# Kernel tuning notes

Hardware: AMD Instinct MI355X
Metric: run time of the kernel (lower is better)

Reference implementation:

```python
import jax, jax.numpy as jnp
import numpy as np

# reformer-enwik8-style config (trimmed to 2 layers, 2 hash rounds)
B, S, D = 2, 4096, 1024          # batch, seq, hidden
H, Dh = 8, 128                   # heads, head dim (H*Dh == D)
R, C, NB = 2, 64, 128            # num hashes, lsh chunk len, num buckets
L, FF, V = 2, 4096, 258          # layers, ffn dim, vocab
EPS = 1e-12
CAUSAL_NEG, SELF_NEG = -1e9, -1e5


def layer_norm(x, g, b):
    mu = x.mean(-1, keepdims=True)
    var = ((x - mu) ** 2).mean(-1, keepdims=True)
    return (x - mu) * jax.lax.rsqrt(var + EPS) * g + b


def lsh_attn(h, Wqk, Wv, Wo, rot):
    # shared query/key projection (Reformer LSH uses tied Q=K)
    qk = (h @ Wqk).reshape(B, S, H, Dh).transpose(0, 2, 1, 3)   # [B,H,S,Dh]
    v = (h @ Wv).reshape(B, S, H, Dh).transpose(0, 2, 1, 3)
    # LSH bucketing via random rotations: rot [H,Dh,R,NB//2]
    rotated = jnp.einsum('bhsd,hdrn->bhrsn', qk, rot)
    buckets = jnp.argmax(jnp.concatenate([rotated, -rotated], -1), axis=-1)  # [B,H,R,S]
    ids = (buckets + jnp.arange(R)[None, None, :, None] * NB).reshape(B, H, R * S)
    pos = jnp.tile(jnp.arange(S), R)
    # stable sort by (bucket, position)
    sticker = jnp.argsort(ids * S + pos[None, None, :], axis=-1)  # [B,H,R*S]
    orig = sticker % S
    gather = lambda t: jnp.take_along_axis(t, orig[..., None], axis=2)
    sq = gather(qk)                                               # [B,H,RS,Dh]
    sv = gather(v)
    # key = len-normalized qk / sqrt(Dh) (HF _len_and_dim_norm)
    sk = sq * jax.lax.rsqrt(jnp.mean(sq * sq, -1, keepdims=True) + 1e-6) / jnp.sqrt(float(Dh))
    nc = R * S // C
    qc = sq.reshape(B, H, nc, C, Dh)
    kc = sk.reshape(B, H, nc, C, Dh)
    vc = sv.reshape(B, H, nc, C, Dh)
    pc = orig.reshape(B, H, nc, C)
    # attend to current chunk + 1 previous chunk (wraparound, as in HF)
    ke = jnp.concatenate([jnp.roll(kc, 1, axis=2), kc], axis=3)   # [B,H,nc,2C,Dh]
    ve = jnp.concatenate([jnp.roll(vc, 1, axis=2), vc], axis=3)
    pe = jnp.concatenate([jnp.roll(pc, 1, axis=2), pc], axis=3)   # [B,H,nc,2C]
    scores = jnp.einsum('bhncd,bhnkd->bhnck', qc, ke)
    qpos, kpos = pc[..., :, None], pe[..., None, :]
    scores = jnp.where(kpos > qpos, CAUSAL_NEG, scores)           # causal (decoder)
    scores = jnp.where(kpos == qpos, SELF_NEG, scores)            # mask self (q==k)
    lse = jax.scipy.special.logsumexp(scores, axis=-1, keepdims=True)
    probs = jnp.exp(scores - lse)
    o = jnp.einsum('bhnck,bhnkd->bhncd', probs, ve).reshape(B, H, R * S, Dh)
    lg = lse.reshape(B, H, R * S)
    undo = jnp.argsort(sticker, axis=-1)
    o = jnp.take_along_axis(o, undo[..., None], axis=2).reshape(B, H, R, S, Dh)
    lg = jnp.take_along_axis(lg, undo, axis=2).reshape(B, H, R, S)
    # combine hash rounds weighted by their logsumexp
    w = jax.nn.softmax(lg, axis=2)[..., None]
    out = (o * w).sum(2)                                          # [B,H,S,Dh]
    out = out.transpose(0, 2, 1, 3).reshape(B, S, H * Dh)
    return out @ Wo


def _forward(x, ln1_g, ln1_b, Wqk, Wv, Wo, rot, ln2_g, ln2_b, W1, b1, W2, b2,
             lnf_g, lnf_b, Wout, bout):
    # reversible residual encoder: x1,x2 start as duplicated hidden states
    x1 = x2 = x
    for l in range(L):
        x1 = x1 + lsh_attn(layer_norm(x2, ln1_g[l], ln1_b[l]), Wqk[l], Wv[l], Wo[l], rot[l])
        x2 = x2 + jax.nn.relu(layer_norm(x1, ln2_g[l], ln2_b[l]) @ W1[l] + b1[l]) @ W2[l] + b2[l]
    hcat = layer_norm(jnp.concatenate([x1, x2], -1), lnf_g, lnf_b)  # [B,S,2D]
    logits = hcat @ Wout + bout
    # F.softmax(x) with no dim on a 3D tensor -> legacy torch dim=0
    return jax.nn.softmax(logits, axis=0)


def setup_inputs() -> dict:
    key = jax.random.key(0)
    ks = jax.random.split(key, 8)
    s = 0.02
    return {
        'x': jax.random.normal(ks[0], (B, S, D), jnp.float32),
        'ln1_g': jnp.ones((L, D), jnp.float32), 'ln1_b': jnp.zeros((L, D), jnp.float32),
        'Wqk': jax.random.normal(ks[1], (L, D, H * Dh), jnp.float32) * s,
        'Wv': jax.random.normal(ks[2], (L, D, H * Dh), jnp.float32) * s,
        'Wo': jax.random.normal(ks[3], (L, H * Dh, D), jnp.float32) * s,
        'rot': jax.random.normal(ks[4], (L, H, Dh, R, NB // 2), jnp.float32),
        'ln2_g': jnp.ones((L, D), jnp.float32), 'ln2_b': jnp.zeros((L, D), jnp.float32),
        'W1': jax.random.normal(ks[5], (L, D, FF), jnp.float32) * s,
        'b1': jnp.zeros((L, FF), jnp.float32),
        'W2': jax.random.normal(ks[6], (L, FF, D), jnp.float32) * s,
        'b2': jnp.zeros((L, D), jnp.float32),
        'lnf_g': jnp.ones((2 * D,), jnp.float32), 'lnf_b': jnp.zeros((2 * D,), jnp.float32),
        'Wout': jax.random.normal(ks[7], (2 * D, V), jnp.float32) * s,
        'bout': jnp.zeros((V,), jnp.float32),
    }


def reference(x, ln1_g, ln1_b, Wqk, Wv, Wo, rot, ln2_g, ln2_b, W1, b1, W2, b2,
              lnf_g, lnf_b, Wout, bout):
    return _forward(x, ln1_g, ln1_b, Wqk, Wv, Wo, rot, ln2_g, ln2_b, W1, b1, W2, b2,
                    lnf_g, lnf_b, Wout, bout)
```

## Files before the change

### kernel.cpp

```cpp
#include <hip/hip_runtime.h>
#include <hip/hip_fp16.h>
#include <math.h>

#define BB 2
#define SS 4096
#define DD 1024
#define HH 8
#define DH 128
#define RR 2
#define CC 64
#define NBUCK 128
#define LL 2
#define FFD 4096
#define VV 258
#define VP 384
#define RS (RR*SS)
#define NC (RS/CC)
#define BH (BB*HH)
#define MROWS (BB*SS)

#define SCF 256.0f
#define DSCF (1.0f/65536.0f)

typedef __attribute__((ext_vector_type(8))) _Float16 v8h;
typedef __attribute__((ext_vector_type(4))) _Float16 v4h;
typedef __attribute__((ext_vector_type(4))) float v4f;

__device__ __forceinline__ void gld16(const void* g, void* l) {
  __builtin_amdgcn_global_load_lds((const __attribute__((address_space(1))) void*)g,
                                   (__attribute__((address_space(3))) void*)l, 16, 0, 0);
}

__device__ __forceinline__ void block_sum2(float& s, float& s2) {
  #pragma unroll
  for (int o = 1; o < 64; o <<= 1) { s += __shfl_xor(s, o); s2 += __shfl_xor(s2, o); }
  __shared__ float rs[4], rq[4];
  int wave = threadIdx.x >> 6;
  if ((threadIdx.x & 63) == 0) { rs[wave] = s; rq[wave] = s2; }
  __syncthreads();
  s  = rs[0] + rs[1] + rs[2] + rs[3];
  s2 = rq[0] + rq[1] + rq[2] + rq[3];
}

__global__ __launch_bounds__(256) void init_x_kernel(const float* __restrict__ x,
                                                     float* __restrict__ x1,
                                                     float* __restrict__ x2) {
  size_t i = (size_t)blockIdx.x * 256 + threadIdx.x;
  float v = x[i];
  x1[i] = v; x2[i] = v;
}

__global__ __launch_bounds__(256) void ln_split_kernel(const float* __restrict__ x,
                                                       const float* __restrict__ g,
                                                       const float* __restrict__ bta,
                                                       _Float16* __restrict__ out) {
  int row = blockIdx.x;
  int t = threadIdx.x;
  float4 xv = ((const float4*)(x + (size_t)row * DD))[t];
  float s  = xv.x + xv.y + xv.z + xv.w;
  float s2 = xv.x*xv.x + xv.y*xv.y + xv.z*xv.z + xv.w*xv.w;
  block_sum2(s, s2);
  float mu   = s * (1.0f / DD);
  float var  = fmaxf(s2 * (1.0f / DD) - mu * mu, 0.0f);
  float rstd = rsqrtf(var + 1e-12f);
  float4 gv = ((const float4*)g)[t];
  float4 bv = ((const float4*)bta)[t];
  float4 sv;
  sv.x = ((xv.x - mu) * rstd * gv.x + bv.x) * SCF;
  sv.y = ((xv.y - mu) * rstd * gv.y + bv.y) * SCF;
  sv.z = ((xv.z - mu) * rstd * gv.z + bv.z) * SCF;
  sv.w = ((xv.w - mu) * rstd * gv.w + bv.w) * SCF;
  v4h h0, h1;
  h0[0]=(_Float16)sv.x; h0[1]=(_Float16)sv.y; h0[2]=(_Float16)sv.z; h0[3]=(_Float16)sv.w;
  h1[0]=(_Float16)(sv.x-(float)h0[0]); h1[1]=(_Float16)(sv.y-(float)h0[1]);
  h1[2]=(_Float16)(sv.z-(float)h0[2]); h1[3]=(_Float16)(sv.w-(float)h0[3]);
  const size_t PLN = (size_t)MROWS * DD;
  size_t base = (size_t)row * DD + t * 4;
  *(v4h*)(out + base) = h0;
  *(v4h*)(out + PLN + base) = h1;
}

__global__ __launch_bounds__(256) void ln_concat_split_kernel(const float* __restrict__ x1,
                                                              const float* __restrict__ x2,
                                                              const float* __restrict__ g,
                                                              const float* __restrict__ bta,
                                                              _Float16* __restrict__ out) {
  int row = blockIdx.x;
  int t = threadIdx.x;
  float4 a = ((const float4*)(x1 + (size_t)row * DD))[t];
  float4 b = ((const float4*)(x2 + (size_t)row * DD))[t];
  float s  = a.x + a.y + a.z + a.w + b.x + b.y + b.z + b.w;
  float s2 = a.x*a.x + a.y*a.y + a.z*a.z + a.w*a.w
           + b.x*b.x + b.y*b.y + b.z*b.z + b.w*b.w;
  block_sum2(s, s2);
  float mu   = s * (1.0f / (2*DD));
  float var  = fmaxf(s2 * (1.0f / (2*DD)) - mu * mu, 0.0f);
  float rstd = rsqrtf(var + 1e-12f);
  float4 g1 = ((const float4*)g)[t];
  float4 b1v = ((const float4*)bta)[t];
  float4 g2 = ((const float4*)g)[256 + t];
  float4 b2v = ((const float4*)bta)[256 + t];
  const size_t PLN = (size_t)MROWS * (2*DD);
  float4 s1, s2v;
  s1.x = ((a.x-mu)*rstd*g1.x + b1v.x)*SCF;  s1.y = ((a.y-mu)*rstd*g1.y + b1v.y)*SCF;
  s1.z = ((a.z-mu)*rstd*g1.z + b1v.z)*SCF;  s1.w = ((a.w-mu)*rstd*g1.w + b1v.w)*SCF;
  s2v.x = ((b.x-mu)*rstd*g2.x + b2v.x)*SCF; s2v.y = ((b.y-mu)*rstd*g2.y + b2v.y)*SCF;
  s2v.z = ((b.z-mu)*rstd*g2.z + b2v.z)*SCF; s2v.w = ((b.w-mu)*rstd*g2.w + b2v.w)*SCF;
  v4h h0, h1;
  size_t base = (size_t)row * (2*DD) + t * 4;
  h0[0]=(_Float16)s1.x; h0[1]=(_Float16)s1.y; h0[2]=(_Float16)s1.z; h0[3]=(_Float16)s1.w;
  h1[0]=(_Float16)(s1.x-(float)h0[0]); h1[1]=(_Float16)(s1.y-(float)h0[1]);
  h1[2]=(_Float16)(s1.z-(float)h0[2]); h1[3]=(_Float16)(s1.w-(float)h0[3]);
  *(v4h*)(out + base) = h0;
  *(v4h*)(out + PLN + base) = h1;
  h0[0]=(_Float16)s2v.x; h0[1]=(_Float16)s2v.y; h0[2]=(_Float16)s2v.z; h0[3]=(_Float16)s2v.w;
  h1[0]=(_Float16)(s2v.x-(float)h0[0]); h1[1]=(_Float16)(s2v.y-(float)h0[1]);
  h1[2]=(_Float16)(s2v.z-(float)h0[2]); h1[3]=(_Float16)(s2v.w-(float)h0[3]);
  *(v4h*)(out + base + DD) = h0;
  *(v4h*)(out + PLN + base + DD) = h1;
}

__global__ __launch_bounds__(256) void wconv_kernel(const float* __restrict__ W,
                                                    _Float16* __restrict__ Wt,
                                                    int K, int N, int Npad, int ldw) {
  __shared__ float tile[32][33];
  int n0 = blockIdx.x * 32, k0 = blockIdx.y * 32;
  int tid = threadIdx.x;
  #pragma unroll
  for (int i = 0; i < 4; i++) {
    int idx = i*256 + tid;
    int kk = idx >> 5, nn = idx & 31;
    float v = 0.0f;
    if (n0 + nn < N) v = W[(size_t)(k0 + kk) * ldw + n0 + nn];
    tile[kk][nn] = v;
  }
  __syncthreads();
  size_t NKs = (size_t)Npad * K;
  #pragma unroll
  for (int i = 0; i < 4; i++) {
    int idx = i*256 + tid;
    int nn = idx >> 5, kk = idx & 31;
    float s = tile[kk][nn] * SCF;
    size_t off = (size_t)(n0 + nn) * K + k0 + kk;
    _Float16 h0 = (_Float16)s;
    _Float16 h1 = (_Float16)(s - (float)h0);
    Wt[off] = h0;
    Wt[NKs + off] = h1;
  }
}

template<int PL, int CMODE, bool BIAS, bool RELU, int NP>
__global__ __launch_bounds__(256) void qgemm_kernel(const _Float16* __restrict__ A,
                                                    const _Float16* __restrict__ Bt,
                                                    const float* __restrict__ bias,
                                                    void* __restrict__ Cv,
                                                    int M, int N, int K,
                                                    size_t aplane, size_t bplane) {
  __shared__ __align__(16) _Float16 As[2*128*32];
  __shared__ __align__(16) _Float16 Bs[2*128*32];
  int tid = threadIdx.x, lane = tid & 63, wave = tid >> 6;
  int m0 = blockIdx.y * 128, n0 = blockIdx.x * 128;
  int wm = (wave & 1) * 64, wn = (wave >> 1) * 64;
  int lm = lane & 15, quad = lane >> 4;
  const int NCH = (PL == 2) ? 8 : 4;
  const int ACH = (PL == 2) ? 16 : 8;
  v4f acc[4][4];
  #pragma unroll
  for (int i = 0; i < 4; i++)
    #pragma unroll
    for (int j = 0; j < 4; j++) acc[i][j] = (v4f)0.0f;

  for (int k0 = 0; k0 < K; k0 += 32) {
    #pragma unroll
    for (int i = 0; i < NCH; i++) {
      int c = wave * NCH + i;
      if (c < ACH) {
        int p = c >> 3, q = c & 7;
        int row = q * 16 + (lane >> 2), col = (lane & 3) * 8;
        gld16(A + (size_t)p * aplane + (size_t)(m0 + row) * K + k0 + col,
              (char*)As + (size_t)c * 1024);
      } else {
        int cb = c - ACH;
        int p = cb >> 3, q = cb & 7;
        int row = q * 16 + (lane >> 2), col = (lane & 3) * 8;
        gld16(Bt + (size_t)p * bplane + (size_t)(n0 + row) * K + k0 + col,
              (char*)Bs + (size_t)cb * 1024);
      }
    }
    __syncthreads();
    v8h a[4][2], b[4][2];
    #pragma unroll
    for (int ni = 0; ni < 4; ni++) {
      int boff = (wn + ni*16 + lm) * 32 + quad * 8;
      b[ni][0] = *(const v8h*)&Bs[boff];
      if (PL == 2) b[ni][1] = *(const v8h*)&Bs[4096 + boff];
    }
    #pragma unroll
    for (int mi = 0; mi < 4; mi++) {
      int aoff = (wm + mi*16 + lm) * 32 + quad * 8;
      a[mi][0] = *(const v8h*)&As[aoff];
      if (PL == 2) a[mi][1] = *(const v8h*)&As[4096 + aoff];
    }
    #pragma unroll
    for (int mi = 0; mi < 4; mi++) {
      #pragma unroll
      for (int ni = 0; ni < 4; ni++) {
        v4f c0 = acc[mi][ni];
        c0 = __builtin_amdgcn_mfma_f32_16x16x32_f16(a[mi][0], b[ni][0], c0, 0, 0, 0);
        if (PL == 2) {
          c0 = __builtin_amdgcn_mfma_f32_16x16x32_f16(a[mi][0], b[ni][1], c0, 0, 0, 0);
          c0 = __builtin_amdgcn_mfma_f32_16x16x32_f16(a[mi][1], b[ni][0], c0, 0, 0, 0);
          if (NP == 4)
            c0 = __builtin_amdgcn_mfma_f32_16x16x32_f16(a[mi][1], b[ni][1], c0, 0, 0, 0);
        }
        acc[mi][ni] = c0;
      }
    }
    __syncthreads();
  }

  float* Cf = (float*)Cv;
  _Float16* Ch = (_Float16*)Cv;
  const size_t cplane = (size_t)M * N;
  #pragma unroll
  for (int mi = 0; mi < 4; mi++) {
    int rbase = m0 + wm + mi*16 + quad*4;
    #pragma unroll
    for (int ni = 0; ni < 4; ni++) {
      int col = n0 + wn + ni*16 + lm;
      float bv = BIAS ? bias[col] : 0.0f;
      #pragma unroll
      for (int r = 0; r < 4; r++) {
        float val = acc[mi][ni][r] * DSCF + bv;
        if (RELU) val = fmaxf(val, 0.0f);
        size_t off = (size_t)(rbase + r) * N + col;
        if (CMODE == 0) Cf[off] = val;
        else if (CMODE == 1) Cf[off] += val;
        else {
          float s = val * SCF;
          _Float16 h0 = (_Float16)s;
          _Float16 h1 = (_Float16)(s - (float)h0);
          Ch[off] = h0;
          Ch[cplane + off] = h1;
        }
      }
    }
  }
}

__global__ __launch_bounds__(256) void rott_kernel(const float* __restrict__ rot,
                                                   _Float16* __restrict__ rotT) {
  int h = blockIdx.x, grp = blockIdx.y;
  const float* rh = rot + (size_t)h * (DH * RR * 64);
  for (int idx = threadIdx.x; idx < 16*128; idx += 256) {
    int rc = grp*16 + (idx >> 7), d = idx & 127;
    int r = rc >> 6, nn = rc & 63;
    float f = rh[(size_t)d * 128 + r * 64 + nn] * SCF;
    _Float16 h0 = (_Float16)f;
    rotT[(size_t)h*32768 + (size_t)rc*128 + d] = h0;
    rotT[(size_t)h*32768 + 16384 + (size_t)rc*128 + d] = (_Float16)(f - (float)h0);
  }
}

__global__ __launch_bounds__(256) void bucket_mfma_kernel(const float* __restrict__ qkb,
                                                          const _Float16* __restrict__ rotT,
                                                          int* __restrict__ ids) {
  __shared__ __align__(16) float Af[128*32];
  __shared__ __align__(16) _Float16 Bs[2*128*32];
  int mtile = blockIdx.x, bh = blockIdx.y;
  int b = bh >> 3, h = bh & 7;
  int tid = threadIdx.x, lane = tid & 63, wave = tid >> 6;
  int wm = (wave & 1) * 64;
  int r = wave >> 1;
  int wn = r * 64;
  int lm = lane & 15, quad = lane >> 4;
  const float* Aq = qkb + ((size_t)b * SS + (size_t)mtile * 128) * DD + h * DH;
  const _Float16* Bq = rotT + (size_t)h * 32768;
  v4f acc[4][4];
  #pragma unroll
  for (int i = 0; i < 4; i++)
    #pragma unroll
    for (int j = 0; j < 4; j++) acc[i][j] = (v4f)0.0f;

  for (int k0 = 0; k0 < 128; k0 += 32) {
    #pragma unroll
    for (int i = 0; i < 8; i++) {
      int c = wave * 8 + i;
      if (c < 16) {
        int slot = c * 64 + lane;
        int row = slot >> 3;
        int c4 = (slot & 7) ^ (row & 7);
        gld16(Aq + (size_t)row * DD + k0 + c4 * 4, (char*)Af + (size_t)c * 1024);
      } else {
        int cb = c - 16;
        int p = cb >> 3, q = cb & 7;
        int row = q * 16 + (lane >> 2), col = (lane & 3) * 8;
        gld16(Bq + (size_t)p * 16384 + (size_t)row * 128 + k0 + col,
              (char*)Bs + (size_t)p * 8192 + (size_t)q * 1024);
      }
    }
    __syncthreads();
    v8h b0[4], b1[4];
    #pragma unroll
    for (int ni = 0; ni < 4; ni++) {
      int boff = (wn + ni*16 + lm) * 32 + quad * 8;
      b0[ni] = *(const v8h*)&Bs[boff];
      b1[ni] = *(const v8h*)&Bs[4096 + boff];
    }
    #pragma unroll
    for (int mi = 0; mi < 4; mi++) {
      int arow = wm + mi*16 + lm;
      int sw = arow & 7;
      float4 fA = *(const float4*)(Af + arow*32 + (((2*quad)     ^ sw) << 2));
      float4 fB = *(const float4*)(Af + arow*32 + (((2*quad + 1) ^ sw) << 2));
      v8h a0, a1;
      float fs[8] = {fA.x*SCF, fA.y*SCF, fA.z*SCF, fA.w*SCF,
                     fB.x*SCF, fB.y*SCF, fB.z*SCF, fB.w*SCF};
      #pragma unroll
      for (int j = 0; j < 8; j++) {
        _Float16 p0 = (_Float16)fs[j];
        a0[j] = p0;
        a1[j] = (_Float16)(fs[j] - (float)p0);
      }
      #pragma unroll
      for (int ni = 0; ni < 4; ni++) {
        v4f c0 = acc[mi][ni];
        c0 = __builtin_amdgcn_mfma_f32_16x16x32_f16(a0, b0[ni], c0, 0, 0, 0);
        c0 = __builtin_amdgcn_mfma_f32_16x16x32_f16(a0, b1[ni], c0, 0, 0, 0);
        c0 = __builtin_amdgcn_mfma_f32_16x16x32_f16(a1, b0[ni], c0, 0, 0, 0);
        c0 = __builtin_amdgcn_mfma_f32_16x16x32_f16(a1, b1[ni], c0, 0, 0, 0);
        acc[mi][ni] = c0;
      }
    }
    __syncthreads();
  }

  #pragma unroll
  for (int mi = 0; mi < 4; mi++) {
    #pragma unroll
    for (int rr = 0; rr < 4; rr++) {
      float mx = acc[mi][0][rr]; int xi = lm;
      float mn = acc[mi][0][rr]; int ni_ = lm;
      #pragma unroll
      for (int ni = 1; ni < 4; ni++) {
        float vv = acc[mi][ni][rr];
        int col = ni*16 + lm;
        if (vv > mx) { mx = vv; xi = col; }
        if (vv < mn) { mn = vv; ni_ = col; }
      }
      #pragma unroll
      for (int o = 1; o < 16; o <<= 1) {
        float ox = __shfl_xor(mx, o); int oxi = __shfl_xor(xi, o);
        if (ox > mx || (ox == mx && oxi < xi)) { mx = ox; xi = oxi; }
        float on = __shfl_xor(mn, o); int oni = __shfl_xor(ni_, o);
        if (on < mn || (on == mn && oni < ni_)) { mn = on; ni_ = oni; }
      }
      if (lm == 0) {
        int bi = (mx >= -mn) ? xi : 64 + ni_;
        int s = mtile*128 + wm + mi*16 + quad*4 + rr;
        ids[((size_t)bh * RR + r) * SS + s] = bi + r * NBUCK;
      }
    }
  }
}

__global__ __launch_bounds__(256) void sort_count_kernel(const int* __restrict__ ids,
                                                         int* __restrict__ counts) {
  int w = blockIdx.x * 4 + (threadIdx.x >> 6);
  int lane = threadIdx.x & 63;
  int bhr = w >> 6, seg = w & 63;
  int id = ids[(size_t)bhr * SS + seg * 64 + lane];
  int bin = id & 127;
  unsigned long long eq = ~0ull;
  #pragma unroll
  for (int bit = 0; bit < 7; bit++) {
    unsigned long long bal = __ballot((bin >> bit) & 1);
    eq &= ((bin >> bit) & 1) ? bal : ~bal;
  }
  int rank = __popcll(eq & ((1ull << lane) - 1ull));
  if (rank == 0)
    counts[((size_t)bhr * 64 + seg) * 128 + bin] = __popcll(eq);
}

__global__ __launch_bounds__(128) void sort_prefix_kernel(int* __restrict__ counts) {
  int bhr = blockIdx.x;
  int bin = threadIdx.x;
  int r = bhr & 1;
  int* cp = counts + (size_t)bhr * 64 * 128;
  int total = 0;
  for (int seg = 0; seg < 64; seg++) total += cp[seg * 128 + bin];
  __shared__ int tot[128];
  tot[bin] = total;
  __syncthreads();
  for (int off = 1; off < 128; off <<= 1) {
    int t = (bin >= off) ? tot[bin - off] : 0;
    __syncthreads();
    tot[bin] += t;
    __syncthreads();
  }
  int run = tot[bin] - total + r * SS;
  for (int seg = 0; seg < 64; seg++) {
    int c = cp[seg * 128 + bin];
    cp[seg * 128 + bin] = run;
    run += c;
  }
}

__global__ __launch_bounds__(256) void sort_scatter_kernel(const int* __restrict__ ids,
                                                           const int* __restrict__ offs,
                                                           int* __restrict__ orig,
                                                           int* __restrict__ undo) {
  int w = blockIdx.x * 4 + (threadIdx.x >> 6);
  int lane = threadIdx.x & 63;
  int bhr = w >> 6, seg = w & 63;
  int s = seg * 64 + lane;
  int id = ids[(size_t)bhr * SS + s];
  int bin = id & 127;
  unsigned long long eq = ~0ull;
  #pragma unroll
  for (int bit = 0; bit < 7; bit++) {
    unsigned long long bal = __ballot((bin >> bit) & 1);
    eq &= ((bin >> bit) & 1) ? bal : ~bal;
  }
  int rank = __popcll(eq & ((1ull << lane) - 1ull));
  int o = offs[((size_t)bhr * 64 + seg) * 128 + bin] + rank;
  int bh = bhr >> 1, r = bhr & 1;
  orig[(size_t)bh * RS + o] = s;
  undo[(size_t)bh * RS + r * SS + s] = o;
}

__global__ __launch_bounds__(256) void rnorm_kernel(const float* __restrict__ qk,
                                                    const int* __restrict__ orig,
                                                    float* __restrict__ rno) {
  int idx = blockIdx.x * 4 + (threadIdx.x >> 6);
  int lane = threadIdx.x & 63;
  int bh = idx >> 13;
  int k = idx & (RS - 1);
  int b = bh >> 3, h = bh & 7;
  int s = orig[(size_t)bh * RS + k];
  const float* row = qk + ((size_t)(b * SS + s)) * DD + h * DH;
  float x0 = row[lane], x1 = row[lane + 64];
  float ss = x0 * x0 + x1 * x1;
  #pragma unroll
  for (int o = 1; o < 64; o <<= 1) ss += __shfl_xor(ss, o);
  if (lane == 0)
    rno[(size_t)bh * RS + k] = rsqrtf(ss * (1.0f / DH) + 1e-6f) * 0.08838834764831845f;
}

template<int PL>
__global__ __launch_bounds__(256) void attn_mfma_kernel(const float* __restrict__ qk,
                                                        const float* __restrict__ v,
                                                        const int* __restrict__ orig,
                                                        const float* __restrict__ rno,
                                                        float* __restrict__ osort,
                                                        float* __restrict__ lg) {
  constexpr int QPs = 64*136, Kps = 32*136, Vps = 128*36;
  constexpr size_t QPB = (size_t)PL * QPs * 2;
  constexpr size_t KVB = (size_t)PL * Vps * 2;
  __shared__ __align__(16) char smem[QPB + KVB + 1024];
  _Float16* QP = (_Float16*)smem;
  _Float16* KV = (_Float16*)(smem + QPB);
  int* kp_lds = (int*)(smem + QPB + KVB);
  int* qp_lds = kp_lds + 128;

  int blk = blockIdx.x;
  int n = blk & (NC - 1), bh = blk >> 7;
  int b = bh >> 3, h = bh & 7;
  int pn = (n + NC - 1) & (NC - 1);
  int tid = threadIdx.x, lane = tid & 63, wave = tid >> 6;
  int lm = lane & 15, quad = lane >> 4;
  const int* origp = orig + (size_t)bh * RS;
  const float* rnp = rno + (size_t)bh * RS;
  const size_t base = (size_t)b * SS * DD + (size_t)h * DH;

  for (int idx = tid; idx < 64*32; idx += 256) {
    int q = idx >> 5, d4 = idx & 31;
    float4 f = *(const float4*)(qk + base + (size_t)origp[n*64+q]*DD + d4*4);
    f.x *= SCF; f.y *= SCF; f.z *= SCF; f.w *= SCF;
    v4h h0; h0[0]=(_Float16)f.x; h0[1]=(_Float16)f.y; h0[2]=(_Float16)f.z; h0[3]=(_Float16)f.w;
    *(v4h*)(QP + q*136 + d4*4) = h0;
    if (PL == 2) {
      v4h h1; h1[0]=(_Float16)(f.x-(float)h0[0]); h1[1]=(_Float16)(f.y-(float)h0[1]);
      h1[2]=(_Float16)(f.z-(float)h0[2]); h1[3]=(_Float16)(f.w-(float)h0[3]);
      *(v4h*)(QP + QPs + q*136 + d4*4) = h1;
    }
  }
  if (tid < 128) kp_lds[tid] = origp[(tid < 64) ? (pn*64 + tid) : (n*64 + tid - 64)];
  else if (tid < 192) qp_lds[tid - 128] = origp[n*64 + tid - 128];

  v4f sc[8];
  #pragma unroll
  for (int j = 0; j < 8; j++) sc[j] = (v4f)0.0f;

  #pragma unroll
  for (int g = 0; g < 4; g++) {
    __syncthreads();
    for (int idx = tid; idx < 32*32; idx += 256) {
      int key = idx >> 5, d4 = idx & 31;
      int kidx = ((g < 2) ? (pn*64 + g*32) : (n*64 + (g-2)*32)) + key;
      float rn = rnp[kidx] * SCF;
      float4 f = *(const float4*)(qk + base + (size_t)origp[kidx]*DD + d4*4);
      f.x *= rn; f.y *= rn; f.z *= rn; f.w *= rn;
      v4h h0; h0[0]=(_Float16)f.x; h0[1]=(_Float16)f.y; h0[2]=(_Float16)f.z; h0[3]=(_Float16)f.w;
      *(v4h*)(KV + key*136 + d4*4) = h0;
      if (PL == 2) {
        v4h h1; h1[0]=(_Float16)(f.x-(float)h0[0]); h1[1]=(_Float16)(f.y-(float)h0[1]);
        h1[2]=(_Float16)(f.z-(float)h0[2]); h1[3]=(_Float16)(f.w-(float)h0[3]);
        *(v4h*)(KV + Kps + key*136 + d4*4) = h1;
      }
    }
    __syncthreads();
    #pragma unroll
    for (int ni = 0; ni < 2; ni++) {
      v4f c0 = sc[g*2 + ni];
      #pragma unroll
      for (int ks = 0; ks < 4; ks++) {
        v8h a0 = *(const v8h*)(QP + (wave*16 + lm)*136 + ks*32 + quad*8);
        v8h b0 = *(const v8h*)(KV + (ni*16 + lm)*136 + ks*32 + quad*8);
        c0 = __builtin_amdgcn_mfma_f32_16x16x32_f16(a0, b0, c0, 0, 0, 0);
        if (PL == 2) {
          v8h a1 = *(const v8h*)(QP + QPs + (wave*16 + lm)*136 + ks*32 + quad*8);
          v8h b1 = *(const v8h*)(KV + Kps + (ni*16 + lm)*136 + ks*32 + quad*8);
          c0 = __builtin_amdgcn_mfma_f32_16x16x32_f16(a0, b1, c0, 0, 0, 0);
          c0 = __builtin_amdgcn_mfma_f32_16x16x32_f16(a1, b0, c0, 0, 0, 0);
          c0 = __builtin_amdgcn_mfma_f32_16x16x32_f16(a1, b1, c0, 0, 0, 0);
        }
      }
      sc[g*2 + ni] = c0;
    }
  }
  __syncthreads();

  int kp_l[8];
  #pragma unroll
  for (int j = 0; j < 8; j++) kp_l[j] = kp_lds[j*16 + lm];

  #pragma unroll
  for (int rr = 0; rr < 4; rr++) {
    int row = wave*16 + quad*4 + rr;
    int qp = qp_lds[row];
    float sv[8];
    #pragma unroll
    for (int j = 0; j < 8; j++) {
      float s = sc[j][rr] * DSCF;
      int kp = kp_l[j];
      sv[j] = (kp > qp) ? -1000000000.0f : ((kp == qp) ? -100000.0f : s);
    }
    float m = sv[0];
    #pragma unroll
    for (int j = 1; j < 8; j++) m = fmaxf(m, sv[j]);
    #pragma unroll
    for (int o = 1; o < 16; o <<= 1) m = fmaxf(m, __shfl_xor(m, o));
    float es[8], S = 0.0f;
    #pragma unroll
    for (int j = 0; j < 8; j++) { es[j] = __expf(sv[j] - m); S += es[j]; }
    #pragma unroll
    for (int o = 1; o < 16; o <<= 1) S += __shfl_xor(S, o);
    float inv = 1.0f / S;
    if (lm == 0) lg[(size_t)bh * RS + n*64 + row] = m + __logf(S);
    #pragma unroll
    for (int j = 0; j < 8; j++) {
      float p = es[j] * inv * SCF;
      _Float16 p0 = (_Float16)p;
      QP[row*136 + j*16 + lm] = p0;
      if (PL == 2) QP[QPs + row*136 + j*16 + lm] = (_Float16)(p - (float)p0);
    }
  }

  v4f oacc[8];
  #pragma unroll
  for (int j = 0; j < 8; j++) oacc[j] = (v4f)0.0f;
  #pragma unroll
  for (int g = 0; g < 4; g++) {
    __syncthreads();
    for (int idx = tid; idx < 32*32; idx += 256) {
      int key = idx >> 5, d4 = idx & 31;
      int kidx = ((g < 2) ? (pn*64 + g*32) : (n*64 + (g-2)*32)) + key;
      float4 f = *(const float4*)(v + base + (size_t)origp[kidx]*DD + d4*4);
      float fs[4] = {f.x*SCF, f.y*SCF, f.z*SCF, f.w*SCF};
      #pragma unroll
      for (int j = 0; j < 4; j++) {
        int d = d4*4 + j;
        _Float16 p0 = (_Float16)fs[j];
        KV[d*36 + key] = p0;
        if (PL == 2) KV[Vps + d*36 + key] = (_Float16)(fs[j] - (float)p0);
      }
    }
    __syncthreads();
    v8h a0 = *(const v8h*)(QP + (wave*16 + lm)*136 + g*32 + quad*8);
    v8h a1;
    if (PL == 2) a1 = *(const v8h*)(QP + QPs + (wave*16 + lm)*136 + g*32 + quad*8);
    #pragma unroll
    for (int dn = 0; dn < 8; dn++) {
      v4h lo0 = *(const v4h*)(KV + (dn*16 + lm)*36 + quad*8);
      v4h hi0 = *(const v4h*)(KV + (dn*16 + lm)*36 + quad*8 + 4);
      v8h b0 = __builtin_shufflevector(lo0, hi0, 0,1,2,3,4,5,6,7);
      v4f c0 = oacc[dn];
      c0 = __builtin_amdgcn_mfma_f32_16x16x32_f16(a0, b0, c0, 0, 0, 0);
      if (PL == 2) {
        v4h lo1 = *(const v4h*)(KV + Vps + (dn*16 + lm)*36 + quad*8);
        v4h hi1 = *(const v4h*)(KV + Vps + (dn*16 + lm)*36 + quad*8 + 4);
        v8h b1 = __builtin_shufflevector(lo1, hi1, 0,1,2,3,4,5,6,7);
        c0 = __builtin_amdgcn_mfma_f32_16x16x32_f16(a0, b1, c0, 0, 0, 0);
        c0 = __builtin_amdgcn_mfma_f32_16x16x32_f16(a1, b0, c0, 0, 0, 0);
        c0 = __builtin_amdgcn_mfma_f32_16x16x32_f16(a1, b1, c0, 0, 0, 0);
      }
      oacc[dn] = c0;
    }
  }

  #pragma unroll
  for (int dn = 0; dn < 8; dn++) {
    #pragma unroll
    for (int rr = 0; rr < 4; rr++) {
      int row = wave*16 + quad*4 + rr;
      osort[((size_t)bh * RS + n*64 + row) * DH + dn*16 + lm] = oacc[dn][rr] * DSCF;
    }
  }
}

__global__ __launch_bounds__(256) void unsort_split_kernel(const float* __restrict__ osort,
                                                           const float* __restrict__ lg,
                                                           const int* __restrict__ undo,
                                                           _Float16* __restrict__ attn) {
  int gid = blockIdx.x * 4 + (threadIdx.x >> 6);
  int lane = threadIdx.x & 63;
  int bh = gid >> 12;
  int s = gid & (SS - 1);
  int b = bh >> 3, h = bh & 7;
  int k0 = undo[(size_t)bh * RS + s];
  int k1 = undo[(size_t)bh * RS + SS + s];
  float l0 = lg[(size_t)bh * RS + k0], l1 = lg[(size_t)bh * RS + k1];
  float m = fmaxf(l0, l1);
  float e0 = __expf(l0 - m), e1 = __expf(l1 - m);
  float inv = 1.0f / (e0 + e1);
  float w0 = e0 * inv, w1 = e1 * inv;
  const float* r0 = osort + ((size_t)bh * RS + k0) * DH;
  const float* r1 = osort + ((size_t)bh * RS + k1) * DH;
  const size_t PLN = (size_t)MROWS * DD;
  _Float16* outp = attn + ((size_t)(b * SS + s)) * DD + h * DH;
  float sA = (w0 * r0[lane]      + w1 * r1[lane])      * SCF;
  float sB = (w0 * r0[lane + 64] + w1 * r1[lane + 64]) * SCF;
  _Float16 a0 = (_Float16)sA, b0 = (_Float16)sB;
  outp[lane] = a0;                 outp[lane + 64] = b0;
  outp[PLN + lane] = (_Float16)(sA - (float)a0);
  outp[PLN + lane + 64] = (_Float16)(sB - (float)b0);
}

__global__ __launch_bounds__(256) void softmax_b_kernel(const float* __restrict__ logits,
                                                        const float* __restrict__ bout,
                                                        float* __restrict__ out) {
  int i = blockIdx.x * 256 + threadIdx.x;
  if (i >= SS * VV) return;
  int s = i / VV, vv = i - s * VV;
  float bvv = bout[vv];
  float l0 = logits[(size_t)s * VP + vv] + bvv;
  float l1 = logits[(size_t)(SS + s) * VP + vv] + bvv;
  float m = fmaxf(l0, l1);
  float e0 = __expf(l0 - m), e1 = __expf(l1 - m);
  float inv = 1.0f / (e0 + e1);
  out[(size_t)s * VV + vv] = e0 * inv;
  out[(size_t)(SS + s) * VV + vv] = e1 * inv;
}

extern "C" void kernel_launch(void* const* d_in, const int* in_sizes, int n_in,
                              void* d_out, int out_size, void* d_ws, size_t ws_size,
                              hipStream_t stream) {
  (void)in_sizes; (void)n_in; (void)out_size; (void)ws_size;
  const float* x     = (const float*)d_in[0];
  const float* ln1_g = (const float*)d_in[1];
  const float* ln1_b = (const float*)d_in[2];
  const float* Wqk   = (const float*)d_in[3];
  const float* Wv    = (const float*)d_in[4];
  const float* Wo    = (const float*)d_in[5];
  const float* rot   = (const float*)d_in[6];
  const float* ln2_g = (const float*)d_in[7];
  const float* ln2_b = (const float*)d_in[8];
  const float* W1    = (const float*)d_in[9];
  const float* b1    = (const float*)d_in[10];
  const float* W2    = (const float*)d_in[11];
  const float* b2    = (const float*)d_in[12];
  const float* lnf_g = (const float*)d_in[13];
  const float* lnf_b = (const float*)d_in[14];
  const float* Wout  = (const float*)d_in[15];
  const float* bout  = (const float*)d_in[16];

  const size_t NX = (size_t)MROWS * DD;
  float* x1 = (float*)d_ws;
  float* x2 = x1 + NX;
  float* h  = x2 + NX;
  _Float16* hs = (_Float16*)h;
  float* pool = h + NX;
  float* qkb   = pool;
  float* vb    = pool + NX;
  float* osort = pool + 2*NX;
  _Float16* ffh = (_Float16*)pool;
  _Float16* hcs = (_Float16*)pool;
  char* wbase = (char*)(pool + 2*NX);
  _Float16* wt = (_Float16*)wbase;
  int* counts = (int*)(wbase + (8u<<20));
  _Float16* rotTs = (_Float16*)(wbase + (10u<<20));
  float* after = pool + 4*NX;
  float* lgb = after;
  float* rno = lgb + (size_t)BH * RS;
  int* orig = (int*)(rno + (size_t)BH * RS);
  int* undo = orig + (size_t)BH * RS;
  int* ids  = undo + (size_t)BH * RS;
  float* logitsP = h;

  const size_t AP_D  = NX;
  const size_t AP_FF = (size_t)MROWS * 2048;
  const size_t BP_D  = (size_t)DD * DD;
  const size_t BP_W1 = (size_t)2048 * DD;
  const size_t BP_W2 = (size_t)DD * 2048;
  const size_t BP_HD = (size_t)VP * 2048;

  init_x_kernel<<<(int)(NX / 256), 256, 0, stream>>>(x, x1, x2);

  for (int l = 0; l < LL; l++) {
    ln_split_kernel<<<MROWS, 256, 0, stream>>>(x2, ln1_g + l*DD, ln1_b + l*DD, hs);

    wconv_kernel<<<dim3(32, 32), 256, 0, stream>>>(Wqk + (size_t)l*DD*DD, wt, DD, DD, DD, DD);
    qgemm_kernel<2,0,false,false,4><<<dim3(8, 64), 256, 0, stream>>>(
        hs, wt, nullptr, qkb, MROWS, DD, DD, AP_D, BP_D);

    wconv_kernel<<<dim3(32, 32), 256, 0, stream>>>(Wv + (size_t)l*DD*DD, wt, DD, DD, DD, DD);
    if (l == 0)
      qgemm_kernel<2,0,false,false,3><<<dim3(8, 64), 256, 0, stream>>>(
          hs, wt, nullptr, vb, MROWS, DD, DD, AP_D, BP_D);
    else
      qgemm_kernel<1,0,false,false,3><<<dim3(8, 64), 256, 0, stream>>>(
          hs, wt, nullptr, vb, MROWS, DD, DD, AP_D, BP_D);

    rott_kernel<<<dim3(8, 8), 256, 0, stream>>>(rot + (size_t)l*HH*DH*RR*64, rotTs);
    bucket_mfma_kernel<<<dim3(32, 16), 256, 0, stream>>>(qkb, rotTs, ids);

    hipMemsetAsync(counts, 0, (size_t)BH * RR * 64 * 128 * sizeof(int), stream);
    sort_count_kernel<<<512, 256, 0, stream>>>(ids, counts);
    sort_prefix_kernel<<<BH*RR, 128, 0, stream>>>(counts);
    sort_scatter_kernel<<<512, 256, 0, stream>>>(ids, counts, orig, undo);

    rnorm_kernel<<<BH*RS/4, 256, 0, stream>>>(qkb, orig, rno);
    if (l == 0)
      attn_mfma_kernel<2><<<BH*NC, 256, 0, stream>>>(qkb, vb, orig, rno, osort, lgb);
    else
      attn_mfma_kernel<1><<<BH*NC, 256, 0, stream>>>(qkb, vb, orig, rno, osort, lgb);
    unsort_split_kernel<<<BH*SS/4, 256, 0, stream>>>(osort, lgb, undo, hs);

    wconv_kernel<<<dim3(32, 32), 256, 0, stream>>>(Wo + (size_t)l*DD*DD, wt, DD, DD, DD, DD);
    if (l == 0)
      qgemm_kernel<2,1,false,false,3><<<dim3(8, 64), 256, 0, stream>>>(
          hs, wt, nullptr, x1, MROWS, DD, DD, AP_D, BP_D);
    else
      qgemm_kernel<1,1,false,false,3><<<dim3(8, 64), 256, 0, stream>>>(
          hs, wt, nullptr, x1, MROWS, DD, DD, AP_D, BP_D);

    ln_split_kernel<<<MROWS, 256, 0, stream>>>(x1, ln2_g + l*DD, ln2_b + l*DD, hs);
    for (int hf = 0; hf < 2; hf++) {
      const float* W1h = W1 + (size_t)l*DD*FFD + (size_t)hf*2048;
      const float* W2h = W2 + (size_t)l*FFD*DD + (size_t)hf*2048*DD;
      _Float16* wt1 = wt;
      _Float16* wt2 = wt + 2u*2097152u;
      wconv_kernel<<<dim3(64, 32), 256, 0, stream>>>(W1h, wt1, DD, 2048, 2048, FFD);
      wconv_kernel<<<dim3(32, 64), 256, 0, stream>>>(W2h, wt2, 2048, DD, DD, DD);
      if (l == 0) {
        qgemm_kernel<2,2,true,true,3><<<dim3(16, 64), 256, 0, stream>>>(
            hs, wt1, b1 + (size_t)l*FFD + hf*2048, ffh, MROWS, 2048, DD, AP_D, BP_W1);
        if (hf == 0)
          qgemm_kernel<2,1,true,false,3><<<dim3(8, 64), 256, 0, stream>>>(
              ffh, wt2, b2 + (size_t)l*DD, x2, MROWS, DD, 2048, AP_FF, BP_W2);
        else
          qgemm_kernel<2,1,false,false,3><<<dim3(8, 64), 256, 0, stream>>>(
              ffh, wt2, nullptr, x2, MROWS, DD, 2048, AP_FF, BP_W2);
      } else {
        qgemm_kernel<1,2,true,true,3><<<dim3(16, 64), 256, 0, stream>>>(
            hs, wt1, b1 + (size_t)l*FFD + hf*2048, ffh, MROWS, 2048, DD, AP_D, BP_W1);
        if (hf == 0)
          qgemm_kernel<1,1,true,false,3><<<dim3(8, 64), 256, 0, stream>>>(
              ffh, wt2, b2 + (size_t)l*DD, x2, MROWS, DD, 2048, AP_FF, BP_W2);
        else
          qgemm_kernel<1,1,false,false,3><<<dim3(8, 64), 256, 0, stream>>>(
              ffh, wt2, nullptr, x2, MROWS, DD, 2048, AP_FF, BP_W2);
      }
    }
  }

  ln_concat_split_kernel<<<MROWS, 256, 0, stream>>>(x1, x2, lnf_g, lnf_b, hcs);
  wconv_kernel<<<dim3(12, 64), 256, 0, stream>>>(Wout, wt, 2*DD, VV, VP, VV);
  qgemm_kernel<1,0,false,false,3><<<dim3(3, 64), 256, 0, stream>>>(
      hcs, wt, nullptr, logitsP, MROWS, VP, 2*DD, AP_FF, BP_HD);
  softmax_b_kernel<<<(SS*VV + 255)/256, 256, 0, stream>>>(logitsP, bout, (float*)d_out);
}
```

Before: 1.851 ms.

## Register-prefetch next K/V chunk in LSH attention and swizzle V LDS layout

The LSH chunk attention kernel now loads the next 32-key K and V tiles into registers while MFMAs run on the current tile, replacing the serial global-load/LDS-store/sync loops with a double-buffered prefetch. Q rows are loaded up front into registers, and key row ids are read from LDS instead of re-reading the orig index from global memory. The transposed V store in LDS gets an XOR swizzle on the key index to cut bank conflicts, and s_setprio is raised around the MFMA sections. This uses more registers, which may lower occupancy, and replaces __syncthreads with raw s_barrier plus manual waitcnt, so correctness depends on those waits covering the outstanding memory operations.

```diff
diff --git a/kernel.cpp b/kernel.cpp
--- a/kernel.cpp
+++ b/kernel.cpp
@@ -473,9 +473,30 @@
   const float* rnp = rno + (size_t)bh * RS;
   const size_t base = (size_t)b * SS * DD + (size_t)h * DH;
 
-  for (int idx = tid; idx < 64*32; idx += 256) {
-    int q = idx >> 5, d4 = idx & 31;
-    float4 f = *(const float4*)(qk + base + (size_t)origp[n*64+q]*DD + d4*4);
+  int d4 = tid & 31;
+  int row0 = tid >> 5;
+  int kb[4] = {pn*64, pn*64 + 32, n*64, n*64 + 32};
+
+  float4 qreg[8];
+  #pragma unroll
+  for (int i = 0; i < 8; i++)
+    qreg[i] = *(const float4*)(qk + base + (size_t)origp[n*64 + row0 + i*8]*DD + d4*4);
+
+  float4 kreg[2][4]; float krn[2][4];
+  #pragma unroll
+  for (int i = 0; i < 4; i++) {
+    int key = row0 + i*8;
+    krn[0][i] = rnp[kb[0] + key];
+    kreg[0][i] = *(const float4*)(qk + base + (size_t)origp[kb[0] + key]*DD + d4*4);
+  }
+
+  if (tid < 128) kp_lds[tid] = origp[(tid < 64) ? (pn*64 + tid) : (n*64 + tid - 64)];
+  else if (tid < 192) qp_lds[tid - 128] = origp[n*64 + tid - 128];
+
+  #pragma unroll
+  for (int i = 0; i < 8; i++) {
+    int q = row0 + i*8;
+    float4 f = qreg[i];
     f.x *= SCF; f.y *= SCF; f.z *= SCF; f.w *= SCF;
     v4h h0; h0[0]=(_Float16)f.x; h0[1]=(_Float16)f.y; h0[2]=(_Float16)f.z; h0[3]=(_Float16)f.w;
     *(v4h*)(QP + q*136 + d4*4) = h0;
@@ -485,8 +506,7 @@
       *(v4h*)(QP + QPs + q*136 + d4*4) = h1;
     }
   }
-  if (tid < 128) kp_lds[tid] = origp[(tid < 64) ? (pn*64 + tid) : (n*64 + tid - 64)];
-  else if (tid < 192) qp_lds[tid - 128] = origp[n*64 + tid - 128];
+  asm volatile("s_waitcnt lgkmcnt(0)" ::: "memory");
 
   v4f sc[8];
   #pragma unroll
@@ -494,12 +514,13 @@
 
   #pragma unroll
   for (int g = 0; g < 4; g++) {
-    __syncthreads();
-    for (int idx = tid; idx < 32*32; idx += 256) {
-      int key = idx >> 5, d4 = idx & 31;
-      int kidx = ((g < 2) ? (pn*64 + g*32) : (n*64 + (g-2)*32)) + key;
-      float rn = rnp[kidx] * SCF;
-      float4 f = *(const float4*)(qk + base + (size_t)origp[kidx]*DD + d4*4);
+    __builtin_amdgcn_s_barrier();
+    int cur = g & 1;
+    #pragma unroll
+    for (int i = 0; i < 4; i++) {
+      int key = row0 + i*8;
+      float rn = krn[cur][i] * SCF;
+      float4 f = kreg[cur][i];
       f.x *= rn; f.y *= rn; f.z *= rn; f.w *= rn;
       v4h h0; h0[0]=(_Float16)f.x; h0[1]=(_Float16)f.y; h0[2]=(_Float16)f.z; h0[3]=(_Float16)f.w;
       *(v4h*)(KV + key*136 + d4*4) = h0;
@@ -509,7 +530,18 @@
         *(v4h*)(KV + Kps + key*136 + d4*4) = h1;
       }
     }
-    __syncthreads();
+    if (g < 3) {
+      #pragma unroll
+      for (int i = 0; i < 4; i++) {
+        int key = row0 + i*8;
+        int rowid = kp_lds[(g+1)*32 + key];
+        krn[cur^1][i] = rnp[kb[g+1] + key];
+        kreg[cur^1][i] = *(const float4*)(qk + base + (size_t)rowid*DD + d4*4);
+      }
+    }
+    asm volatile("s_waitcnt lgkmcnt(0)" ::: "memory");
+    __builtin_amdgcn_s_barrier();
+    __builtin_amdgcn_s_setprio(1);
     #pragma unroll
     for (int ni = 0; ni < 2; ni++) {
       v4f c0 = sc[g*2 + ni];
@@ -528,8 +560,18 @@
       }
       sc[g*2 + ni] = c0;
     }
-  }
-  __syncthreads();
+    __builtin_amdgcn_s_setprio(0);
+  }
+
+  float4 vreg[2][4];
+  #pragma unroll
+  for (int i = 0; i < 4; i++) {
+    int key = row0 + i*8;
+    int rowid = kp_lds[key];
+    vreg[0][i] = *(const float4*)(v + base + (size_t)rowid*DD + d4*4);
+  }
+
+  __builtin_amdgcn_s_barrier();
 
   int kp_l[8];
   #pragma unroll
@@ -572,34 +614,48 @@
   for (int j = 0; j < 8; j++) oacc[j] = (v4f)0.0f;
   #pragma unroll
   for (int g = 0; g < 4; g++) {
-    __syncthreads();
-    for (int idx = tid; idx < 32*32; idx += 256) {
-      int key = idx >> 5, d4 = idx & 31;
-      int kidx = ((g < 2) ? (pn*64 + g*32) : (n*64 + (g-2)*32)) + key;
-      float4 f = *(const float4*)(v + base + (size_t)origp[kidx]*DD + d4*4);
+    __builtin_amdgcn_s_barrier();
+    int cur = g & 1;
+    int xbs = (d4 & 7) << 2;
+    #pragma unroll
+    for (int i = 0; i < 4; i++) {
+      int keyS = (row0 + i*8) ^ xbs;
+      float4 f = vreg[cur][i];
       float fs[4] = {f.x*SCF, f.y*SCF, f.z*SCF, f.w*SCF};
       #pragma unroll
       for (int j = 0; j < 4; j++) {
         int d = d4*4 + j;
         _Float16 p0 = (_Float16)fs[j];
-        KV[d*36 + key] = p0;
-        if (PL == 2) KV[Vps + d*36 + key] = (_Float16)(fs[j] - (float)p0);
-      }
-    }
-    __syncthreads();
+        KV[d*36 + keyS] = p0;
+        if (PL == 2) KV[Vps + d*36 + keyS] = (_Float16)(fs[j] - (float)p0);
+      }
+    }
+    if (g < 3) {
+      #pragma unroll
+      for (int i = 0; i < 4; i++) {
+        int key = row0 + i*8;
+        int rowid = kp_lds[(g+1)*32 + key];
+        vreg[cur^1][i] = *(const float4*)(v + base + (size_t)rowid*DD + d4*4);
+      }
+    }
+    asm volatile("s_waitcnt lgkmcnt(0)" ::: "memory");
+    __builtin_amdgcn_s_barrier();
+    __builtin_amdgcn_s_setprio(1);
     v8h a0 = *(const v8h*)(QP + (wave*16 + lm)*136 + g*32 + quad*8);
     v8h a1;
     if (PL == 2) a1 = *(const v8h*)(QP + QPs + (wave*16 + lm)*136 + g*32 + quad*8);
     #pragma unroll
     for (int dn = 0; dn < 8; dn++) {
-      v4h lo0 = *(const v4h*)(KV + (dn*16 + lm)*36 + quad*8);
-      v4h hi0 = *(const v4h*)(KV + (dn*16 + lm)*36 + quad*8 + 4);
+      int d = dn*16 + lm;
+      int klo = (quad*8) ^ (((d >> 2) & 7) << 2);
+      v4h lo0 = *(const v4h*)(KV + d*36 + klo);
+      v4h hi0 = *(const v4h*)(KV + d*36 + (klo ^ 4));
       v8h b0 = __builtin_shufflevector(lo0, hi0, 0,1,2,3,4,5,6,7);
       v4f c0 = oacc[dn];
       c0 = __builtin_amdgcn_mfma_f32_16x16x32_f16(a0, b0, c0, 0, 0, 0);
       if (PL == 2) {
-        v4h lo1 = *(const v4h*)(KV + Vps + (dn*16 + lm)*36 + quad*8);
-        v4h hi1 = *(const v4h*)(KV + Vps + (dn*16 + lm)*36 + quad*8 + 4);
+        v4h lo1 = *(const v4h*)(KV + Vps + d*36 + klo);
+        v4h hi1 = *(const v4h*)(KV + Vps + d*36 + (klo ^ 4));
         v8h b1 = __builtin_shufflevector(lo1, hi1, 0,1,2,3,4,5,6,7);
         c0 = __builtin_amdgcn_mfma_f32_16x16x32_f16(a0, b1, c0, 0, 0, 0);
         c0 = __builtin_amdgcn_mfma_f32_16x16x32_f16(a1, b0, c0, 0, 0, 0);
@@ -607,6 +663,7 @@
       }
       oacc[dn] = c0;
     }
+    __builtin_amdgcn_s_setprio(0);
   }
 
   #pragma unroll
```

Measured after the change: 1.772 ms. 1.04x faster.
